# Kernel tuning notes

Hardware: AMD Instinct MI355X
Metric: run time of the kernel (lower is better)

Reference implementation:

```python
import jax, jax.numpy as jnp
import numpy as np

CH = 1280
HEADS = 8
HEAD_DIM = 160
INNER = HEADS * HEAD_DIM  # 1280


def setup_inputs() -> dict:
    key = jax.random.key(0)
    ks = jax.random.split(key, 6)
    s = 1.0 / np.sqrt(CH)
    return {
        "hidden_states": jax.random.normal(ks[0], (2, 4096, CH), dtype=jnp.float32),
        "w_q": jax.random.normal(ks[1], (CH, INNER), dtype=jnp.float32) * s,
        "w_k": jax.random.normal(ks[2], (CH, INNER), dtype=jnp.float32) * s,
        "w_v": jax.random.normal(ks[3], (CH, INNER), dtype=jnp.float32) * s,
        "w_out": jax.random.normal(ks[4], (INNER, CH), dtype=jnp.float32) * (1.0 / np.sqrt(INNER)),
        "b_out": jax.random.normal(ks[5], (CH,), dtype=jnp.float32) * 0.01,
    }


def reference(hidden_states, w_q, w_k, w_v, w_out, b_out):
    B, S, C = hidden_states.shape
    scale = 1.0 / np.sqrt(HEAD_DIM)
    # self-attention: context = hidden_states
    q = (hidden_states @ w_q).reshape(B, S, HEADS, HEAD_DIM)
    k = (hidden_states @ w_k).reshape(B, S, HEADS, HEAD_DIM)
    v = (hidden_states @ w_v).reshape(B, S, HEADS, HEAD_DIM)
    # [B, H, S, S] explicit score matrix (matches original non-flash path)
    scores = jnp.einsum("bqhd,bkhd->bhqk", q, k) * scale
    attn = jax.nn.softmax(scores, axis=-1)
    out = jnp.einsum("bhqk,bkhd->bqhd", attn, v).reshape(B, S, INNER)
    return out @ w_out + b_out
```

## Files before the change

kernel.cpp:

```cpp
#include <hip/hip_runtime.h>
#include <hip/hip_bf16.h>
#include <stdint.h>


using bf16x8 = __attribute__((ext_vector_type(8))) short;
using f32x4  = __attribute__((ext_vector_type(4))) float;
using f32x16 = __attribute__((ext_vector_type(16))) float;

__device__ __forceinline__ short f2bf(float f) {
    union { float f; uint32_t u; } v; v.f = f;
    uint32_t r = v.u + 0x7fffu + ((v.u >> 16) & 1u);
    return (short)(r >> 16);
}

__device__ __forceinline__ void async16(const short* g, short* l) {
    __builtin_amdgcn_global_load_lds(
        (const __attribute__((address_space(1))) void*)g,
        (__attribute__((address_space(3))) void*)l, 16, 0, 0);
}

__global__ __launch_bounds__(256) void cast_hs(
    const float* __restrict__ hs, short* __restrict__ out)
{
    int i = (blockIdx.x * 256 + threadIdx.x) * 4;
    float4 v = *(const float4*)&hs[i];
    short4 s; s.x = f2bf(v.x); s.y = f2bf(v.y); s.z = f2bf(v.z); s.w = f2bf(v.w);
    *(short4*)&out[i] = s;
}

__global__ __launch_bounds__(256) void transpose_w(
    const float* __restrict__ w0, const float* __restrict__ w1,
    const float* __restrict__ w2, const float* __restrict__ w3,
    short* __restrict__ wqkvT, short* __restrict__ woutT)
{
    __shared__ float tile[32][33];
    int z = blockIdx.z;
    const float* src = (z == 0) ? w0 : (z == 1) ? w1 : (z == 2) ? w2 : w3;
    short* dst = (z == 3) ? woutT : (wqkvT + (long)z * 1280 * 1280);
    int k0 = blockIdx.x * 32, n0 = blockIdx.y * 32;
    int t = threadIdx.x, r = t >> 5, c = t & 31;
#pragma unroll
    for (int i = 0; i < 4; i++)
        tile[r + i * 8][c] = src[(long)(k0 + r + i * 8) * 1280 + n0 + c];
    __syncthreads();
#pragma unroll
    for (int i = 0; i < 4; i++)
        dst[(long)(n0 + r + i * 8) * 1280 + k0 + c] = f2bf(tile[c][r + i * 8]);
}

__global__ __launch_bounds__(256) void transpose_v(
    const short* __restrict__ v, short* __restrict__ vt)
{
    __shared__ short tile[32][33];
    int s0 = blockIdx.x * 32, d0 = blockIdx.y * 32;
    long bh = blockIdx.z;
    const short* src = v + bh * 4096 * 160;
    short* dst = vt + bh * 160 * 4096;
    int t = threadIdx.x, r = t >> 5, c = t & 31;
#pragma unroll
    for (int i = 0; i < 4; i++)
        tile[r + i * 8][c] = src[(s0 + r + i * 8) * 160 + d0 + c];
    __syncthreads();
#pragma unroll
    for (int i = 0; i < 4; i++)
        dst[(d0 + r + i * 8) * 4096 + s0 + c] = tile[c][r + i * 8];
}

template <int MODE>
__global__ __launch_bounds__(256, 3) void gemm_k(
    const short* __restrict__ A, const short* __restrict__ BT,
    short* __restrict__ q_h, short* __restrict__ k_h, short* __restrict__ v_h,
    float* __restrict__ outp, const float* __restrict__ bias)
{
    __shared__ __align__(16) short A_lds[128 * 64];
    __shared__ __align__(16) short B_lds[128 * 64];

    int t = threadIdx.x, wave = t >> 6, lane = t & 63;
    int quad = lane >> 4, l15 = lane & 15, h7 = l15 & 7;
    int wr = wave >> 1, wc = wave & 1;
    int m0 = blockIdx.y * 128, n0 = blockIdx.x * 128;

    f32x4 acc[4][4] = {};

    for (int kt = 0; kt < 1280; kt += 64) {
        __syncthreads();
#pragma unroll
        for (int i = 0; i < 4; i++) {
            int chunk = wave * 4 + i;
            int c = chunk * 64 + lane;
            int row = c >> 3, j = (c & 7) ^ (row & 7);
            async16(A  + (long)(m0 + row) * 1280 + kt + j * 8, A_lds + chunk * 512);
            async16(BT + (long)(n0 + row) * 1280 + kt + j * 8, B_lds + chunk * 512);
        }
        __syncthreads();

#pragma unroll
        for (int dk = 0; dk < 2; dk++) {
            bf16x8 a[4], b[4];
#pragma unroll
            for (int mi = 0; mi < 4; mi++) {
                int row = wr * 64 + mi * 16 + l15;
                a[mi] = *(const bf16x8*)&A_lds[row * 64 + ((dk * 4 + quad) ^ h7) * 8];
            }
#pragma unroll
            for (int ni = 0; ni < 4; ni++) {
                int row = wc * 64 + ni * 16 + l15;
                b[ni] = *(const bf16x8*)&B_lds[row * 64 + ((dk * 4 + quad) ^ h7) * 8];
            }
#pragma unroll
            for (int mi = 0; mi < 4; mi++)
#pragma unroll
                for (int ni = 0; ni < 4; ni++)
                    acc[mi][ni] = __builtin_amdgcn_mfma_f32_16x16x32_bf16(
                        a[mi], b[ni], acc[mi][ni], 0, 0, 0);
        }
    }

    const float SL2E = 0.07905694150420949f * 1.4426950408889634f;
#pragma unroll
    for (int mi = 0; mi < 4; mi++) {
#pragma unroll
        for (int ni = 0; ni < 4; ni++) {
#pragma unroll
            for (int r = 0; r < 4; r++) {
                int gr = m0 + wr * 64 + mi * 16 + quad * 4 + r;
                int gc = n0 + wc * 64 + ni * 16 + l15;
                float val = acc[mi][ni][r];
                if (MODE == 0) {
                    int which = gc / 1280;
                    int c1 = gc - which * 1280;
                    int hh = c1 / 160, d = c1 - hh * 160;
                    int b_ = gr >> 12, s = gr & 4095;
                    long addr = (((long)(b_ * 8 + hh)) * 4096 + s) * 160 + d;
                    if (which == 0) val *= SL2E;
                    short* dst = (which == 0) ? q_h : (which == 1) ? k_h : v_h;
                    dst[addr] = f2bf(val);
                } else {
                    outp[(long)gr * 1280 + gc] = val + bias[gc];
                }
            }
        }
    }
}

__global__ __launch_bounds__(256, 2) void flash_k(
    const short* __restrict__ q_h, const short* __restrict__ k_h,
    const short* __restrict__ v_t, short* __restrict__ attn_out)
{
    __shared__ __align__(16) short Ks128[64 * 128];
    __shared__ __align__(16) short Ks32 [64 * 32];
    __shared__ __align__(16) short Vs   [160 * 64];

    int t = threadIdx.x, wave = t >> 6, lane = t & 63;
    int l31 = lane & 31, hi = lane >> 5;
    int qt = blockIdx.x;
    long bh = blockIdx.y;
    int b = (int)(bh >> 3), h = (int)(bh & 7);

    bf16x8 qf[10];
    {
        const short* qg = q_h + (bh * 4096 + qt * 128 + wave * 32 + l31) * 160;
#pragma unroll
        for (int dk = 0; dk < 10; dk++)
            qf[dk] = *(const bf16x8*)&qg[dk * 16 + hi * 8];
    }

    auto stageK = [&](int k0) {
        const short* kg = k_h + (bh * 4096 + k0) * 160;
#pragma unroll
        for (int i = 0; i < 4; i++) {
            int chunk = wave * 4 + i;
            int c = chunk * 64 + lane;
            int row = c >> 4, j = (c & 15) ^ (row & 7);
            async16(kg + row * 160 + j * 8, Ks128 + chunk * 512);
        }
        {
            int row = wave * 16 + (lane >> 2);
            int j = (lane & 3) ^ ((lane >> 3) & 3);
            async16(kg + row * 160 + 128 + j * 8, Ks32 + wave * 512);
        }
    };
    auto stageV = [&](int k0) {
#pragma unroll
        for (int i = 0; i < 5; i++) {
            int chunk = wave * 5 + i;
            int c = chunk * 64 + lane;
            int row = c >> 3, j = (c & 7) ^ (row & 7);
            async16(v_t + (bh * 160 + row) * 4096 + k0 + j * 8, Vs + chunk * 512);
        }
    };

    f32x16 o[5] = {};
    float lacc = 0.f;

    stageK(0);
    stageV(0);
    asm volatile("s_waitcnt vmcnt(5)" ::: "memory");
    asm volatile("s_waitcnt lgkmcnt(0)" ::: "memory");
    __builtin_amdgcn_s_barrier();

    for (int k0 = 0; k0 < 4096; k0 += 64) {
        uint32_t pw[4][4];

#pragma unroll
        for (int kt = 0; kt < 2; kt++) {
            f32x16 s = {};
            __builtin_amdgcn_s_setprio(1);
#pragma unroll
            for (int dk = 0; dk < 8; dk++) {
                bf16x8 ka = *(const bf16x8*)
                    &Ks128[(kt * 32 + l31) * 128 + (((dk * 2 + hi) ^ (l31 & 7)) * 8)];
                s = __builtin_amdgcn_mfma_f32_32x32x16_bf16(ka, qf[dk], s, 0, 0, 0);
            }
#pragma unroll
            for (int dk = 8; dk < 10; dk++) {
                bf16x8 ka = *(const bf16x8*)
                    &Ks32[(kt * 32 + l31) * 32 + ((((dk - 8) * 2 + hi) ^ ((l31 >> 1) & 3)) * 8)];
                s = __builtin_amdgcn_mfma_f32_32x32x16_bf16(ka, qf[dk], s, 0, 0, 0);
            }
            __builtin_amdgcn_s_setprio(0);

            uint32_t u[4][2];
#pragma unroll
            for (int rg = 0; rg < 4; rg++) {
                float e0 = exp2f(s[rg * 4 + 0] - 16.f);
                float e1 = exp2f(s[rg * 4 + 1] - 16.f);
                float e2 = exp2f(s[rg * 4 + 2] - 16.f);
                float e3 = exp2f(s[rg * 4 + 3] - 16.f);
                uint32_t pk0, pk1;
                asm("v_cvt_pk_bf16_f32 %0, %1, %2" : "=v"(pk0) : "v"(e0), "v"(e1));
                asm("v_cvt_pk_bf16_f32 %0, %1, %2" : "=v"(pk1) : "v"(e2), "v"(e3));
                u[rg][0] = pk0; u[rg][1] = pk1;
                float r0 = __uint_as_float(pk0 << 16)
                         + __uint_as_float(pk0 & 0xffff0000u);
                float r1 = __uint_as_float(pk1 << 16)
                         + __uint_as_float(pk1 & 0xffff0000u);
                lacc += (r0 + r1);
            }
#pragma unroll
            for (int ksl = 0; ksl < 2; ksl++)
#pragma unroll
                for (int c = 0; c < 2; c++) {
                    auto r = __builtin_amdgcn_permlane32_swap(
                        u[2 * ksl][c], u[2 * ksl + 1][c], false, false);
                    pw[kt * 2 + ksl][c]     = (uint32_t)r[0];
                    pw[kt * 2 + ksl][c + 2] = (uint32_t)r[1];
                }
        }

        asm volatile("s_waitcnt vmcnt(0)" ::: "memory");
        asm volatile("s_waitcnt lgkmcnt(0)" ::: "memory");
        __builtin_amdgcn_s_barrier();

        if (k0 + 64 < 4096) stageK(k0 + 64);

        __builtin_amdgcn_s_setprio(1);
#pragma unroll
        for (int ks = 0; ks < 4; ks++) {
            union { uint32_t w[4]; bf16x8 v; } ap;
            ap.w[0] = pw[ks][0]; ap.w[1] = pw[ks][1];
            ap.w[2] = pw[ks][2]; ap.w[3] = pw[ks][3];
#pragma unroll
            for (int ct = 0; ct < 5; ct++) {
                int row = ct * 32 + l31;
                bf16x8 bv = *(const bf16x8*)
                    &Vs[row * 64 + (((ks * 2 + hi) ^ (row & 7)) * 8)];
                o[ct] = __builtin_amdgcn_mfma_f32_32x32x16_bf16(ap.v, bv, o[ct], 0, 0, 0);
            }
        }
        __builtin_amdgcn_s_setprio(0);

        asm volatile("s_waitcnt vmcnt(0)" ::: "memory");
        asm volatile("s_waitcnt lgkmcnt(0)" ::: "memory");
        __builtin_amdgcn_s_barrier();

        if (k0 + 64 < 4096) stageV(k0 + 64);
    }

    float lsum = lacc + __shfl_xor(lacc, 32);
    float inv = 1.0f / lsum;
    float iv[16];
#pragma unroll
    for (int r = 0; r < 16; r++)
        iv[r] = __shfl(inv, (r & 3) + 8 * (r >> 2) + 4 * hi);

#pragma unroll
    for (int ct = 0; ct < 5; ct++)
#pragma unroll
        for (int r = 0; r < 16; r++) {
            int crow = (r & 3) + 8 * (r >> 2) + 4 * hi;
            int gr = b * 4096 + qt * 128 + wave * 32 + crow;
            int gc = h * 160 + ct * 32 + l31;
            attn_out[(long)gr * 1280 + gc] = f2bf(o[ct][r] * iv[r]);
        }
}

extern "C" void kernel_launch(void* const* d_in, const int* in_sizes, int n_in,
                              void* d_out, int out_size, void* d_ws, size_t ws_size,
                              hipStream_t stream)
{
    const float* hs = (const float*)d_in[0];
    const float* wq = (const float*)d_in[1];
    const float* wk = (const float*)d_in[2];
    const float* wv = (const float*)d_in[3];
    const float* wo = (const float*)d_in[4];
    const float* bo = (const float*)d_in[5];
    float* out = (float*)d_out;

    char* ws = (char*)d_ws;
    short* wqkvT = (short*)(ws + 0);
    short* woutT = (short*)(ws + 9830400);
    short* q_h   = (short*)(ws + 13107200);
    short* k_h   = (short*)(ws + 34078720);
    short* v_t   = (short*)(ws + 55050240);
    short* v_h   = (short*)(ws + 76021760);
    short* attn  = v_h;
    short* hs_bf = v_t;

    cast_hs<<<10240, 256, 0, stream>>>(hs, hs_bf);
    transpose_w<<<dim3(40, 40, 4), 256, 0, stream>>>(wq, wk, wv, wo, wqkvT, woutT);
    gemm_k<0><<<dim3(30, 64), 256, 0, stream>>>(hs_bf, wqkvT, q_h, k_h, v_h,
                                                nullptr, nullptr);
    transpose_v<<<dim3(128, 5, 16), 256, 0, stream>>>(v_h, v_t);
    flash_k<<<dim3(32, 16), 256, 0, stream>>>(q_h, k_h, v_t, attn);
    gemm_k<1><<<dim3(10, 64), 256, 0, stream>>>(attn, woutT, nullptr, nullptr,
                                                nullptr, out, bo);
}
```

Measured before the change: 464.6 us.

## Split QK accumulator chains, fix Ks32 swizzle, sum fp32 exps directly

Splits the QK^T MFMA chain into two independent accumulators (sa, sb) that are added at the end, which breaks the serial dependency between back-to-back MFMAs. Changes the XOR swizzle for the 32-wide K tail in LDS to mix in higher row bits, aiming to remove bank conflicts on the Ks32 reads. Sums the row denominator from the fp32 exponentials instead of from the bf16-rounded values, which saves the unpack ALU ops. In exchange it adds an extra vector add and 16 more accumulator registers, and the denominator no longer exactly matches the bf16 probabilities used in PV.

After: 453.7 us. -2.3%, faster.

```diff
diff --git a/kernel.cpp b/kernel.cpp
--- a/kernel.cpp
+++ b/kernel.cpp
@@ -176,7 +176,8 @@
         }
         {
             int row = wave * 16 + (lane >> 2);
-            int j = (lane & 3) ^ ((lane >> 3) & 3);
+            int r31 = row & 31;
+            int j = (lane & 3) ^ (((r31 >> 1) & 3) ^ ((r31 >> 3) & 3));
             async16(kg + row * 160 + 128 + j * 8, Ks32 + wave * 512);
         }
     };
@@ -192,6 +193,7 @@
 
     f32x16 o[5] = {};
     float lacc = 0.f;
+    int sk31 = ((l31 >> 1) & 3) ^ ((l31 >> 3) & 3);
 
     stageK(0);
     stageV(0);
@@ -204,21 +206,27 @@
 
 #pragma unroll
         for (int kt = 0; kt < 2; kt++) {
-            f32x16 s = {};
+            f32x16 sa = {}, sb = {};
             __builtin_amdgcn_s_setprio(1);
 #pragma unroll
-            for (int dk = 0; dk < 8; dk++) {
-                bf16x8 ka = *(const bf16x8*)
+            for (int dk = 0; dk < 8; dk += 2) {
+                bf16x8 ka0 = *(const bf16x8*)
                     &Ks128[(kt * 32 + l31) * 128 + (((dk * 2 + hi) ^ (l31 & 7)) * 8)];
-                s = __builtin_amdgcn_mfma_f32_32x32x16_bf16(ka, qf[dk], s, 0, 0, 0);
-            }
-#pragma unroll
-            for (int dk = 8; dk < 10; dk++) {
-                bf16x8 ka = *(const bf16x8*)
-                    &Ks32[(kt * 32 + l31) * 32 + ((((dk - 8) * 2 + hi) ^ ((l31 >> 1) & 3)) * 8)];
-                s = __builtin_amdgcn_mfma_f32_32x32x16_bf16(ka, qf[dk], s, 0, 0, 0);
+                bf16x8 ka1 = *(const bf16x8*)
+                    &Ks128[(kt * 32 + l31) * 128 + ((((dk + 1) * 2 + hi) ^ (l31 & 7)) * 8)];
+                sa = __builtin_amdgcn_mfma_f32_32x32x16_bf16(ka0, qf[dk],     sa, 0, 0, 0);
+                sb = __builtin_amdgcn_mfma_f32_32x32x16_bf16(ka1, qf[dk + 1], sb, 0, 0, 0);
+            }
+            {
+                bf16x8 ka8 = *(const bf16x8*)
+                    &Ks32[(kt * 32 + l31) * 32 + (((0 * 2 + hi) ^ sk31) * 8)];
+                bf16x8 ka9 = *(const bf16x8*)
+                    &Ks32[(kt * 32 + l31) * 32 + (((1 * 2 + hi) ^ sk31) * 8)];
+                sa = __builtin_amdgcn_mfma_f32_32x32x16_bf16(ka8, qf[8], sa, 0, 0, 0);
+                sb = __builtin_amdgcn_mfma_f32_32x32x16_bf16(ka9, qf[9], sb, 0, 0, 0);
             }
             __builtin_amdgcn_s_setprio(0);
+            f32x16 s = sa + sb;
 
             uint32_t u[4][2];
 #pragma unroll
@@ -231,11 +239,7 @@
                 asm("v_cvt_pk_bf16_f32 %0, %1, %2" : "=v"(pk0) : "v"(e0), "v"(e1));
                 asm("v_cvt_pk_bf16_f32 %0, %1, %2" : "=v"(pk1) : "v"(e2), "v"(e3));
                 u[rg][0] = pk0; u[rg][1] = pk1;
-                float r0 = __uint_as_float(pk0 << 16)
-                         + __uint_as_float(pk0 & 0xffff0000u);
-                float r1 = __uint_as_float(pk1 << 16)
-                         + __uint_as_float(pk1 & 0xffff0000u);
-                lacc += (r0 + r1);
+                lacc += (e0 + e1) + (e2 + e3);
             }
 #pragma unroll
             for (int ksl = 0; ksl < 2; ksl++)
```

## Split flash attention KV range across two wave groups with LDS reduction

Applied to the files above, without the earlier changes.

Flash kernel now uses 512 threads per block: two groups of four waves each process half of the key/value sequence for the same 128 query rows, with per-group LDS buffers and 32-key steps. At the end the partial outputs and row sums are combined through LDS before normalisation and store. The last 32 head dims of K are loaded straight into registers rather than staged in LDS, and the row-sum now accumulates fp32 exponentials instead of bf16-rounded ones. This doubles the waves per CU with the aim of better latency hiding and MFMA occupancy, at the cost of smaller per-iteration work, more barriers, and an added cross-group reduction.

New measurement: 498.6 us. 1.07x slower.

```diff
diff --git a/kernel.cpp b/kernel.cpp
--- a/kernel.cpp
+++ b/kernel.cpp
@@ -143,51 +143,59 @@
     }
 }
 
-__global__ __launch_bounds__(256, 2) void flash_k(
+__global__ __launch_bounds__(512, 2) void flash_k(
     const short* __restrict__ q_h, const short* __restrict__ k_h,
     const short* __restrict__ v_t, short* __restrict__ attn_out)
 {
-    __shared__ __align__(16) short Ks128[64 * 128];
-    __shared__ __align__(16) short Ks32 [64 * 32];
-    __shared__ __align__(16) short Vs   [160 * 64];
+    __shared__ __align__(16) short LDS[2 * 9216];
 
     int t = threadIdx.x, wave = t >> 6, lane = t & 63;
     int l31 = lane & 31, hi = lane >> 5;
+    int qw = wave & 3, kvh = wave >> 2;
     int qt = blockIdx.x;
     long bh = blockIdx.y;
     int b = (int)(bh >> 3), h = (int)(bh & 7);
 
+    short* Kb128 = LDS + kvh * 9216;
+    short* Vb    = Kb128 + 4096;
+    long kbase = bh * 4096 + kvh * 2048;
+
     bf16x8 qf[10];
     {
-        const short* qg = q_h + (bh * 4096 + qt * 128 + wave * 32 + l31) * 160;
+        const short* qg = q_h + (bh * 4096 + qt * 128 + qw * 32 + l31) * 160;
 #pragma unroll
         for (int dk = 0; dk < 10; dk++)
             qf[dk] = *(const bf16x8*)&qg[dk * 16 + hi * 8];
     }
 
     auto stageK = [&](int k0) {
-        const short* kg = k_h + (bh * 4096 + k0) * 160;
-#pragma unroll
-        for (int i = 0; i < 4; i++) {
-            int chunk = wave * 4 + i;
+        const short* kg = k_h + (kbase + k0) * 160;
+#pragma unroll
+        for (int i = 0; i < 2; i++) {
+            int chunk = qw * 2 + i;
             int c = chunk * 64 + lane;
             int row = c >> 4, j = (c & 15) ^ (row & 7);
-            async16(kg + row * 160 + j * 8, Ks128 + chunk * 512);
-        }
-        {
-            int row = wave * 16 + (lane >> 2);
-            int j = (lane & 3) ^ ((lane >> 3) & 3);
-            async16(kg + row * 160 + 128 + j * 8, Ks32 + wave * 512);
-        }
+            async16(kg + row * 160 + j * 8, Kb128 + chunk * 512);
+        }
+    };
+    auto stageVc = [&](int chunk, int k0) {
+        int c = chunk * 64 + lane;
+        int row = c >> 2;
+        int sw = (row & 3) ^ ((row >> 2) & 3);
+        int j = (c & 3) ^ sw;
+        async16(v_t + (bh * 160 + row) * 4096 + kvh * 2048 + k0 + j * 8,
+                Vb + chunk * 512);
     };
     auto stageV = [&](int k0) {
-#pragma unroll
-        for (int i = 0; i < 5; i++) {
-            int chunk = wave * 5 + i;
-            int c = chunk * 64 + lane;
-            int row = c >> 3, j = (c & 7) ^ (row & 7);
-            async16(v_t + (bh * 160 + row) * 4096 + k0 + j * 8, Vs + chunk * 512);
-        }
+        stageVc(qw * 2 + 0, k0);
+        stageVc(qw * 2 + 1, k0);
+        if (qw < 2) stageVc(8 + qw, k0);
+    };
+    bf16x8 kt8, kt9;
+    auto loadTail = [&](int k0) {
+        const short* kgt = k_h + (kbase + k0 + l31) * 160;
+        kt8 = *(const bf16x8*)&kgt[128 + hi * 8];
+        kt9 = *(const bf16x8*)&kgt[144 + hi * 8];
     };
 
     f32x16 o[5] = {};
@@ -195,76 +203,68 @@
 
     stageK(0);
     stageV(0);
-    asm volatile("s_waitcnt vmcnt(5)" ::: "memory");
-    asm volatile("s_waitcnt lgkmcnt(0)" ::: "memory");
+    loadTail(0);
+    asm volatile("s_waitcnt vmcnt(2)" ::: "memory");
     __builtin_amdgcn_s_barrier();
 
-    for (int k0 = 0; k0 < 4096; k0 += 64) {
-        uint32_t pw[4][4];
-
-#pragma unroll
-        for (int kt = 0; kt < 2; kt++) {
-            f32x16 s = {};
-            __builtin_amdgcn_s_setprio(1);
-#pragma unroll
-            for (int dk = 0; dk < 8; dk++) {
-                bf16x8 ka = *(const bf16x8*)
-                    &Ks128[(kt * 32 + l31) * 128 + (((dk * 2 + hi) ^ (l31 & 7)) * 8)];
-                s = __builtin_amdgcn_mfma_f32_32x32x16_bf16(ka, qf[dk], s, 0, 0, 0);
-            }
-#pragma unroll
-            for (int dk = 8; dk < 10; dk++) {
-                bf16x8 ka = *(const bf16x8*)
-                    &Ks32[(kt * 32 + l31) * 32 + ((((dk - 8) * 2 + hi) ^ ((l31 >> 1) & 3)) * 8)];
-                s = __builtin_amdgcn_mfma_f32_32x32x16_bf16(ka, qf[dk], s, 0, 0, 0);
-            }
-            __builtin_amdgcn_s_setprio(0);
-
-            uint32_t u[4][2];
-#pragma unroll
-            for (int rg = 0; rg < 4; rg++) {
-                float e0 = exp2f(s[rg * 4 + 0] - 16.f);
-                float e1 = exp2f(s[rg * 4 + 1] - 16.f);
-                float e2 = exp2f(s[rg * 4 + 2] - 16.f);
-                float e3 = exp2f(s[rg * 4 + 3] - 16.f);
-                uint32_t pk0, pk1;
-                asm("v_cvt_pk_bf16_f32 %0, %1, %2" : "=v"(pk0) : "v"(e0), "v"(e1));
-                asm("v_cvt_pk_bf16_f32 %0, %1, %2" : "=v"(pk1) : "v"(e2), "v"(e3));
-                u[rg][0] = pk0; u[rg][1] = pk1;
-                float r0 = __uint_as_float(pk0 << 16)
-                         + __uint_as_float(pk0 & 0xffff0000u);
-                float r1 = __uint_as_float(pk1 << 16)
-                         + __uint_as_float(pk1 & 0xffff0000u);
-                lacc += (r0 + r1);
-            }
-#pragma unroll
-            for (int ksl = 0; ksl < 2; ksl++)
-#pragma unroll
-                for (int c = 0; c < 2; c++) {
-                    auto r = __builtin_amdgcn_permlane32_swap(
-                        u[2 * ksl][c], u[2 * ksl + 1][c], false, false);
-                    pw[kt * 2 + ksl][c]     = (uint32_t)r[0];
-                    pw[kt * 2 + ksl][c + 2] = (uint32_t)r[1];
-                }
-        }
+    for (int k0 = 0; k0 < 2048; k0 += 32) {
+        f32x16 s = {};
+        __builtin_amdgcn_s_setprio(1);
+#pragma unroll
+        for (int dk = 0; dk < 8; dk++) {
+            bf16x8 ka = *(const bf16x8*)
+                &Kb128[l31 * 128 + (((dk * 2 + hi) ^ (l31 & 7)) * 8)];
+            s = __builtin_amdgcn_mfma_f32_32x32x16_bf16(ka, qf[dk], s, 0, 0, 0);
+        }
+        s = __builtin_amdgcn_mfma_f32_32x32x16_bf16(kt8, qf[8], s, 0, 0, 0);
+        s = __builtin_amdgcn_mfma_f32_32x32x16_bf16(kt9, qf[9], s, 0, 0, 0);
+        __builtin_amdgcn_s_setprio(0);
+
+        uint32_t u[4][2];
+#pragma unroll
+        for (int rg = 0; rg < 4; rg++) {
+            float e0 = exp2f(s[rg * 4 + 0] - 16.f);
+            float e1 = exp2f(s[rg * 4 + 1] - 16.f);
+            float e2 = exp2f(s[rg * 4 + 2] - 16.f);
+            float e3 = exp2f(s[rg * 4 + 3] - 16.f);
+            uint32_t pk0, pk1;
+            asm("v_cvt_pk_bf16_f32 %0, %1, %2" : "=v"(pk0) : "v"(e0), "v"(e1));
+            asm("v_cvt_pk_bf16_f32 %0, %1, %2" : "=v"(pk1) : "v"(e2), "v"(e3));
+            u[rg][0] = pk0; u[rg][1] = pk1;
+            lacc += (e0 + e1) + (e2 + e3);
+        }
+        uint32_t pw[2][4];
+#pragma unroll
+        for (int ksl = 0; ksl < 2; ksl++)
+#pragma unroll
+            for (int c = 0; c < 2; c++) {
+                auto r = __builtin_amdgcn_permlane32_swap(
+                    u[2 * ksl][c], u[2 * ksl + 1][c], false, false);
+                pw[ksl][c]     = (uint32_t)r[0];
+                pw[ksl][c + 2] = (uint32_t)r[1];
+            }
 
         asm volatile("s_waitcnt vmcnt(0)" ::: "memory");
         asm volatile("s_waitcnt lgkmcnt(0)" ::: "memory");
         __builtin_amdgcn_s_barrier();
 
-        if (k0 + 64 < 4096) stageK(k0 + 64);
+        if (k0 + 32 < 2048) {
+            stageK(k0 + 32);
+            loadTail(k0 + 32);
+        }
 
         __builtin_amdgcn_s_setprio(1);
 #pragma unroll
-        for (int ks = 0; ks < 4; ks++) {
+        for (int ks = 0; ks < 2; ks++) {
             union { uint32_t w[4]; bf16x8 v; } ap;
             ap.w[0] = pw[ks][0]; ap.w[1] = pw[ks][1];
             ap.w[2] = pw[ks][2]; ap.w[3] = pw[ks][3];
 #pragma unroll
             for (int ct = 0; ct < 5; ct++) {
                 int row = ct * 32 + l31;
+                int sw = (row & 3) ^ ((row >> 2) & 3);
                 bf16x8 bv = *(const bf16x8*)
-                    &Vs[row * 64 + (((ks * 2 + hi) ^ (row & 7)) * 8)];
+                    &Vb[row * 32 + (((ks * 2 + hi) ^ sw) * 8)];
                 o[ct] = __builtin_amdgcn_mfma_f32_32x32x16_bf16(ap.v, bv, o[ct], 0, 0, 0);
             }
         }
@@ -274,25 +274,65 @@
         asm volatile("s_waitcnt lgkmcnt(0)" ::: "memory");
         __builtin_amdgcn_s_barrier();
 
-        if (k0 + 64 < 4096) stageV(k0 + 64);
+        if (k0 + 32 < 2048) stageV(k0 + 32);
     }
 
     float lsum = lacc + __shfl_xor(lacc, 32);
-    float inv = 1.0f / lsum;
-    float iv[16];
-#pragma unroll
-    for (int r = 0; r < 16; r++)
-        iv[r] = __shfl(inv, (r & 3) + 8 * (r >> 2) + 4 * hi);
-
-#pragma unroll
-    for (int ct = 0; ct < 5; ct++)
-#pragma unroll
-        for (int r = 0; r < 16; r++) {
-            int crow = (r & 3) + 8 * (r >> 2) + 4 * hi;
-            int gr = b * 4096 + qt * 128 + wave * 32 + crow;
-            int gc = h * 160 + ct * 32 + l31;
-            attn_out[(long)gr * 1280 + gc] = f2bf(o[ct][r] * iv[r]);
-        }
+
+    float* exL = (float*)LDS;
+    if (kvh == 1 && hi == 0) exL[qw * 32 + l31] = lsum;
+    asm volatile("s_waitcnt lgkmcnt(0)" ::: "memory");
+    __builtin_amdgcn_s_barrier();
+    float lsum_o = 0.f;
+    if (kvh == 0) lsum_o = exL[qw * 32 + l31];
+    asm volatile("s_waitcnt lgkmcnt(0)" ::: "memory");
+    __builtin_amdgcn_s_barrier();
+
+    float* exO = (float*)LDS;
+#define XCHUNK(P0, P1)                                                         \
+    if (kvh == 1) {                                                            \
+        _Pragma("unroll")                                                      \
+        for (int p = P0; p < P1; p++) {                                        \
+            float4 v4 = { o[p >> 2][(p & 3) * 4 + 0], o[p >> 2][(p & 3) * 4 + 1], \
+                          o[p >> 2][(p & 3) * 4 + 2], o[p >> 2][(p & 3) * 4 + 3] }; \
+            *(float4*)&exO[(p - P0) * 1024 + qw * 256 + lane * 4] = v4;        \
+        }                                                                      \
+    }                                                                          \
+    asm volatile("s_waitcnt lgkmcnt(0)" ::: "memory");                         \
+    __builtin_amdgcn_s_barrier();                                              \
+    if (kvh == 0) {                                                            \
+        _Pragma("unroll")                                                      \
+        for (int p = P0; p < P1; p++) {                                        \
+            float4 v4 = *(const float4*)&exO[(p - P0) * 1024 + qw * 256 + lane * 4]; \
+            o[p >> 2][(p & 3) * 4 + 0] += v4.x; o[p >> 2][(p & 3) * 4 + 1] += v4.y; \
+            o[p >> 2][(p & 3) * 4 + 2] += v4.z; o[p >> 2][(p & 3) * 4 + 3] += v4.w; \
+        }                                                                      \
+    }                                                                          \
+    asm volatile("s_waitcnt lgkmcnt(0)" ::: "memory");                         \
+    __builtin_amdgcn_s_barrier();
+
+    XCHUNK(0, 8)
+    XCHUNK(8, 16)
+    XCHUNK(16, 20)
+#undef XCHUNK
+
+    if (kvh == 0) {
+        float inv = 1.0f / (lsum + lsum_o);
+        float iv[16];
+#pragma unroll
+        for (int r = 0; r < 16; r++)
+            iv[r] = __shfl(inv, (r & 3) + 8 * (r >> 2) + 4 * hi);
+
+#pragma unroll
+        for (int ct = 0; ct < 5; ct++)
+#pragma unroll
+            for (int r = 0; r < 16; r++) {
+                int crow = (r & 3) + 8 * (r >> 2) + 4 * hi;
+                int gr = b * 4096 + qt * 128 + qw * 32 + crow;
+                int gc = h * 160 + ct * 32 + l31;
+                attn_out[(long)gr * 1280 + gc] = f2bf(o[ct][r] * iv[r]);
+            }
+    }
 }
 
 extern "C" void kernel_launch(void* const* d_in, const int* in_sizes, int n_in,
@@ -322,7 +362,7 @@
     gemm_k<0><<<dim3(30, 64), 256, 0, stream>>>(hs_bf, wqkvT, q_h, k_h, v_h,
                                                 nullptr, nullptr);
     transpose_v<<<dim3(128, 5, 16), 256, 0, stream>>>(v_h, v_t);
-    flash_k<<<dim3(32, 16), 256, 0, stream>>>(q_h, k_h, v_t, attn);
+    flash_k<<<dim3(32, 16), 512, 0, stream>>>(q_h, k_h, v_t, attn);
     gemm_k<1><<<dim3(10, 64), 256, 0, stream>>>(attn, woutT, nullptr, nullptr,
                                                 nullptr, out, bo);
 }
```
